# Performance work log

Measured on AMD Instinct MI355X. Metric: run time of the kernel, lower is better.

Reference implementation:

```python
import jax, jax.numpy as jnp
import numpy as np
import math

EMBED_DIM = 1024
NUM_HEADS = 16
HEAD_DIM = EMBED_DIM // NUM_HEADS
SCALE = 1.0 / math.sqrt(HEAD_DIM)


def setup_inputs() -> dict:
    key = jax.random.key(0)
    ks = jax.random.split(key, 11)
    B, S, E = 4, 2048, EMBED_DIM
    lim = 1.0 / math.sqrt(E)
    def lin(k):
        kw, kb = jax.random.split(k)
        W = jax.random.uniform(kw, (E, E), jnp.float32, -lim, lim)
        b = jax.random.uniform(kb, (E,), jnp.float32, -lim, lim)
        return W, b
    Wq, bq = lin(ks[0])
    Wk, bk = lin(ks[1])
    Wv, bv = lin(ks[2])
    Wo, bo = lin(ks[3])
    query = jax.random.normal(ks[4], (B, S, E), jnp.float32)
    key_t = jax.random.normal(ks[5], (B, S, E), jnp.float32)
    value = jax.random.normal(ks[6], (B, S, E), jnp.float32)
    return {"query": query, "key": key_t, "value": value,
            "Wq": Wq, "bq": bq, "Wk": Wk, "bk": bk,
            "Wv": Wv, "bv": bv, "Wo": Wo, "bo": bo}


def reference(query, key, value, Wq, bq, Wk, bk, Wv, bv, Wo, bo):
    B, S, E = query.shape
    H, D = NUM_HEADS, HEAD_DIM
    # nn.Linear: x @ W^T + b; reshape to (B, H, S, D)
    def proj(x, W, b):
        return (x @ W.T + b).reshape(B, S, H, D).transpose(0, 2, 1, 3)
    q = proj(query, Wq, bq)
    k = proj(key, Wk, bk)
    v = proj(value, Wv, bv)
    scores = jnp.einsum('bhsd,bhtd->bhst', q, k) * SCALE  # [B,H,S,S]
    attn = jax.nn.softmax(scores, axis=-1)
    # dropout is identity in eval/reference mode
    attended = jnp.einsum('bhst,bhtd->bhsd', attn, v)
    attended = attended.transpose(0, 2, 1, 3).reshape(B, S, E)
    out = attended @ Wo.T + bo
    return out, attn
```

## Files before the change

### kernel.cpp

```cpp
#include <hip/hip_runtime.h>
#include <hip/hip_bf16.h>

typedef __attribute__((ext_vector_type(8))) short short8;
typedef __attribute__((ext_vector_type(4))) float f32x4;
typedef unsigned short u16;
typedef unsigned int u32;

#define AS1 __attribute__((address_space(1)))
#define AS3 __attribute__((address_space(3)))

__device__ __forceinline__ void cp16(const void* g, void* l) {
  __builtin_amdgcn_global_load_lds((const AS1 u32*)g, (AS3 u32*)l, 16, 0, 0);
}

__device__ __forceinline__ u16 f2bf(float x) {
  union { float f; unsigned u; } c; c.f = x;
  unsigned u = c.u;
  unsigned r = (u + 0x7fffu + ((u >> 16) & 1u)) >> 16;
  return (u16)r;
}

__device__ __forceinline__ u32 pk2bf(float a, float b) {
  __hip_bfloat162 h = __float22bfloat162_rn(float2{a, b});
  union { __hip_bfloat162 h; u32 u; } c; c.h = h; return c.u;
}

__device__ __forceinline__ short8 cvt8(float4 x0, float4 x1) {
  short8 v;
  v[0]=(short)f2bf(x0.x); v[1]=(short)f2bf(x0.y); v[2]=(short)f2bf(x0.z); v[3]=(short)f2bf(x0.w);
  v[4]=(short)f2bf(x1.x); v[5]=(short)f2bf(x1.y); v[6]=(short)f2bf(x1.z); v[7]=(short)f2bf(x1.w);
  return v;
}

__global__ __launch_bounds__(256) void cvt_all(
    const float* __restrict__ q, const float* __restrict__ k, const float* __restrict__ v,
    const float* __restrict__ wq, const float* __restrict__ wk,
    const float* __restrict__ wv, const float* __restrict__ wo,
    u16* __restrict__ Xb, u16* __restrict__ Wb)
{
  const int TOT = 3670016;
  for (int c = blockIdx.x * 256 + threadIdx.x; c < TOT; c += gridDim.x * 256) {
    const float* s; u16* d;
    if (c < 3145728) {
      int z = c >> 20, off = c & 1048575;
      s = ((z == 0) ? q : (z == 1) ? k : v) + (size_t)off * 8;
      d = Xb + (size_t)c * 8;
    } else {
      int wc = c - 3145728;
      int z = wc >> 17, off = wc & 131071;
      s = ((z == 0) ? wq : (z == 1) ? wk : (z == 2) ? wv : wo) + (size_t)off * 8;
      d = Wb + (size_t)wc * 8;
    }
    float4 a = ((const float4*)s)[0], b = ((const float4*)s)[1];
    *(short8*)d = cvt8(a, b);
  }
}

template<int SWAP>
__device__ __forceinline__ void gemm_core_bf16(const u16* __restrict__ A,
                                               const u16* __restrict__ B,
                                               u16* As, u16* Bs,
                                               f32x4 acc[4][4])
{
  const int tid = threadIdx.x;
  const int lane = tid & 63, wid = tid >> 6;
  const int lo = lane & 15, hi = lane >> 4;
  const int wr0 = (wid >> 1) * 64, wc0 = (wid & 1) * 64;

  for (int k0 = 0; k0 < 1024; k0 += 64) {
    __syncthreads();
#pragma unroll
    for (int it = 0; it < 4; ++it) {
      int idx = it * 256 + tid;
      int row = idx >> 3, slot = idx & 7;
      cp16(A + (size_t)row * 1024 + k0 + slot * 8, As + (size_t)idx * 8);
      cp16(B + (size_t)row * 1024 + k0 + slot * 8, Bs + (size_t)idx * 8);
    }
    __syncthreads();
#pragma unroll
    for (int kk = 0; kk < 2; ++kk) {
      short8 af[4], bfr[4];
      int slot = kk * 4 + hi;
#pragma unroll
      for (int i = 0; i < 4; ++i)
        af[i] = *(const short8*)(&As[(wr0 + i * 16 + lo) * 64 + slot * 8]);
#pragma unroll
      for (int j = 0; j < 4; ++j)
        bfr[j] = *(const short8*)(&Bs[(wc0 + j * 16 + lo) * 64 + slot * 8]);
#pragma unroll
      for (int i = 0; i < 4; ++i)
#pragma unroll
        for (int j = 0; j < 4; ++j)
          acc[i][j] = SWAP
            ? __builtin_amdgcn_mfma_f32_16x16x32_bf16(bfr[j], af[i], acc[i][j], 0, 0, 0)
            : __builtin_amdgcn_mfma_f32_16x16x32_bf16(af[i], bfr[j], acc[i][j], 0, 0, 0);
    }
  }
}

__global__ __launch_bounds__(256) void gemm_qkv(
    const u16* __restrict__ Xb, const u16* __restrict__ Wb,
    const float* __restrict__ bq, const float* __restrict__ bk, const float* __restrict__ bv,
    u16* __restrict__ Qh, u16* __restrict__ Kh, u16* __restrict__ Vt)
{
  __shared__ __align__(16) u16 As[128 * 64];
  __shared__ __align__(16) u16 Bs[128 * 64];
  const int bid = blockIdx.x;
  const int w = (bid & 7) * 192 + (bid >> 3);
  const int z = w / 512, r = w % 512;
  const int bm0 = (r >> 3) * 128, bn0 = (r & 7) * 128;
  const u16* A = Xb + (size_t)z * 8388608 + (size_t)bm0 * 1024;
  const u16* W = Wb + (size_t)z * 1048576 + (size_t)bn0 * 1024;
  const float* bias = (z == 0) ? bq : (z == 1) ? bk : bv;

  f32x4 acc[4][4] = {};
  if (z < 2) gemm_core_bf16<0>(A, W, As, Bs, acc);
  else       gemm_core_bf16<1>(A, W, As, Bs, acc);

  const int lane = threadIdx.x & 63, wid = threadIdx.x >> 6;
  const int lo = lane & 15, hi = lane >> 4;
  const int wr0 = (wid >> 1) * 64, wc0 = (wid & 1) * 64;

  if (z < 2) {
    u16* out = (z == 0) ? Qh : Kh;
    const float sc = (z == 0) ? 0.125f * 1.44269504088896f : 1.0f;
#pragma unroll
    for (int j = 0; j < 4; ++j) {
      int n = bn0 + wc0 + j * 16 + lo;
      float bb = bias[n];
      int h = n >> 6, d = n & 63;
#pragma unroll
      for (int i = 0; i < 4; ++i)
#pragma unroll
        for (int r2 = 0; r2 < 4; ++r2) {
          int m = bm0 + wr0 + i * 16 + hi * 4 + r2;
          int b = m >> 11, s = m & 2047;
          float v = (acc[i][j][r2] + bb) * sc;
          out[(((size_t)(b * 16 + h)) * 2048 + s) * 64 + d] = f2bf(v);
        }
    }
  } else {
#pragma unroll
    for (int j = 0; j < 4; ++j) {
#pragma unroll
      for (int r2 = 0; r2 < 4; ++r2) {
        int n = bn0 + wc0 + j * 16 + hi * 4 + r2;
        float bb = bias[n];
        int h = n >> 6, d = n & 63;
#pragma unroll
        for (int i = 0; i < 4; ++i) {
          int m = bm0 + wr0 + i * 16 + lo;
          int b = m >> 11, s = m & 2047;
          Vt[(((size_t)(b * 16 + h)) * 64 + d) * 2048 + s] = f2bf(acc[i][j][r2] + bb);
        }
      }
    }
  }
}

__global__ __launch_bounds__(256) void gemm_out(
    const u16* __restrict__ ATT, const u16* __restrict__ Wo,
    const float* __restrict__ bo, float* __restrict__ out)
{
  __shared__ __align__(16) u16 As[128 * 64];
  __shared__ __align__(16) u16 Bs[128 * 64];
  const int bid = blockIdx.x;
  const int w = (bid & 7) * 64 + (bid >> 3);
  const int bm0 = (w >> 3) * 128, bn0 = (w & 7) * 128;
  f32x4 acc[4][4] = {};
  gemm_core_bf16<0>(ATT + (size_t)bm0 * 1024, Wo + (size_t)bn0 * 1024, As, Bs, acc);

  const int lane = threadIdx.x & 63, wid = threadIdx.x >> 6;
  const int lo = lane & 15, hi = lane >> 4;
  const int wr0 = (wid >> 1) * 64, wc0 = (wid & 1) * 64;
#pragma unroll
  for (int j = 0; j < 4; ++j) {
    int n = bn0 + wc0 + j * 16 + lo;
    float bb = bo[n];
#pragma unroll
    for (int i = 0; i < 4; ++i)
#pragma unroll
      for (int r = 0; r < 4; ++r) {
        int m = bm0 + wr0 + i * 16 + hi * 4 + r;
        out[(size_t)m * 1024 + n] = acc[i][j][r] + bb;
      }
  }
}

#define C2 11.5415603f
__global__ __launch_bounds__(256) void attn_fused(
    const u16* __restrict__ Qh, const u16* __restrict__ Kh,
    const u16* __restrict__ Vt, float* __restrict__ attnOut,
    u16* __restrict__ ATT)
{
  __shared__ __align__(16) u16 Ks[64 * 64];
  __shared__ __align__(16) u16 Vs[64 * 64];
  __shared__ __align__(16) u16 Ps[64 * 64];
  const int tid = threadIdx.x, lane = tid & 63, wid = tid >> 6;
  const int lo = lane & 15, hi = lane >> 4;
  const int bid = blockIdx.x;
  const int xcd = bid & 7, idx = bid >> 3;
  const int bh = xcd * 8 + (idx >> 5);
  const int q0 = (idx & 31) * 64;
  const int wq0 = wid * 16;
  const int qr = wq0 + lo;

  const u16* Qg  = Qh + ((size_t)bh * 2048 + q0) * 64;
  const u16* Kg0 = Kh + (size_t)bh * 2048 * 64;
  const u16* Vg0 = Vt + (size_t)bh * 64 * 2048;

  short8 qa[2];
#pragma unroll
  for (int kk = 0; kk < 2; ++kk)
    qa[kk] = *(const short8*)(Qg + qr * 64 + (kk * 4 + hi) * 8);

  float lsum = 0.f;
  for (int kt2 = 0; kt2 < 16; ++kt2) {
    int t0 = kt2 * 128;
    __syncthreads();
#pragma unroll
    for (int it = 0; it < 4; ++it) {
      int i2 = it * 256 + tid;
      int row = i2 >> 3, slot = i2 & 7;
      short8 v = *(const short8*)(Kg0 + (size_t)(t0 + row) * 64 + slot * 8);
      if (it < 2) *(short8*)(&Ks[row * 64 + ((slot ^ (row & 7)) << 3)]) = v;
      else        *(short8*)(&Vs[(row - 64) * 64 + ((slot ^ (row & 7)) << 3)]) = v;
    }
    __syncthreads();
#pragma unroll
    for (int half = 0; half < 2; ++half) {
      const u16* Kb = half ? Vs : Ks;
      f32x4 sc[4] = {};
#pragma unroll
      for (int kk = 0; kk < 2; ++kk) {
        int slot = kk * 4 + hi;
#pragma unroll
        for (int j = 0; j < 4; ++j) {
          int row = j * 16 + lo;
          short8 kb = *(const short8*)(&Kb[row * 64 + ((slot ^ (row & 7)) << 3)]);
          sc[j] = __builtin_amdgcn_mfma_f32_16x16x32_bf16(kb, qa[kk], sc[j], 0, 0, 0);
        }
      }
#pragma unroll
      for (int j = 0; j < 4; ++j)
#pragma unroll
        for (int r = 0; r < 4; ++r) lsum += __builtin_amdgcn_exp2f(sc[j][r] - C2);
    }
  }
  lsum += __shfl_xor(lsum, 16);
  lsum += __shfl_xor(lsum, 32);
  const float shift2 = C2 + __builtin_amdgcn_logf(lsum);

  f32x4 oacc[4] = {};
  for (int kt = 0; kt < 32; ++kt) {
    int t0 = kt * 64;
    __syncthreads();
#pragma unroll
    for (int it = 0; it < 2; ++it) {
      int i2 = it * 256 + tid;
      int row = i2 >> 3, slot = i2 & 7;
      short8 v = *(const short8*)(Kg0 + (size_t)(t0 + row) * 64 + slot * 8);
      *(short8*)(&Ks[row * 64 + ((slot ^ (row & 7)) << 3)]) = v;
      short8 w = *(const short8*)(Vg0 + (size_t)row * 2048 + t0 + slot * 8);
      *(short8*)(&Vs[row * 64 + ((slot ^ (row & 7)) << 3)]) = w;
    }
    __syncthreads();
    f32x4 sc[4] = {};
#pragma unroll
    for (int kk = 0; kk < 2; ++kk) {
      int slot = kk * 4 + hi;
#pragma unroll
      for (int j = 0; j < 4; ++j) {
        int row = j * 16 + lo;
        short8 kb = *(const short8*)(&Ks[row * 64 + ((slot ^ (row & 7)) << 3)]);
        sc[j] = __builtin_amdgcn_mfma_f32_16x16x32_bf16(kb, qa[kk], sc[j], 0, 0, 0);
      }
    }
    float p[4][4];
#pragma unroll
    for (int j = 0; j < 4; ++j)
#pragma unroll
      for (int r = 0; r < 4; ++r) p[j][r] = __builtin_amdgcn_exp2f(sc[j][r] - shift2);

    float* aOut = attnOut + ((size_t)bh * 2048 + q0 + qr) * 2048 + t0 + hi * 4;
#pragma unroll
    for (int j = 0; j < 4; ++j) {
      f32x4 f4;
      f4[0] = p[j][0]; f4[1] = p[j][1]; f4[2] = p[j][2]; f4[3] = p[j][3];
      __builtin_nontemporal_store(f4, (f32x4*)(aOut + j * 16));
    }
#pragma unroll
    for (int j = 0; j < 4; ++j) {
      int byte = (qr * 128 + j * 32 + hi * 8) ^ ((qr & 7) << 4);
      uint2 uu; uu.x = pk2bf(p[j][0], p[j][1]); uu.y = pk2bf(p[j][2], p[j][3]);
      *(uint2*)((char*)Ps + byte) = uu;
    }
#pragma unroll
    for (int c = 0; c < 2; ++c) {
      int byte = (qr * 128 + c * 64 + hi * 16) ^ ((qr & 7) << 4);
      short8 pa = *(const short8*)((char*)Ps + byte);
      int slot = c * 4 + hi;
#pragma unroll
      for (int j = 0; j < 4; ++j) {
        int vrow = j * 16 + lo;
        short8 vb = *(const short8*)(&Vs[vrow * 64 + ((slot ^ (vrow & 7)) << 3)]);
        oacc[j] = __builtin_amdgcn_mfma_f32_16x16x32_bf16(pa, vb, oacc[j], 0, 0, 0);
      }
    }
  }
  const int b = bh >> 4, h = bh & 15;
#pragma unroll
  for (int j = 0; j < 4; ++j)
#pragma unroll
    for (int r = 0; r < 4; ++r) {
      int ql = wq0 + hi * 4 + r;
      int d = j * 16 + lo;
      size_t row = (size_t)b * 2048 + q0 + ql;
      ATT[row * 1024 + h * 64 + d] = f2bf(oacc[j][r]);
    }
}

extern "C" void kernel_launch(void* const* d_in, const int* in_sizes, int n_in,
                              void* d_out, int out_size, void* d_ws, size_t ws_size,
                              hipStream_t stream) {
  const float* query = (const float*)d_in[0];
  const float* key   = (const float*)d_in[1];
  const float* value = (const float*)d_in[2];
  const float* Wq = (const float*)d_in[3];
  const float* bq = (const float*)d_in[4];
  const float* Wk = (const float*)d_in[5];
  const float* bk = (const float*)d_in[6];
  const float* Wv = (const float*)d_in[7];
  const float* bv = (const float*)d_in[8];
  const float* Wo = (const float*)d_in[9];
  const float* bo = (const float*)d_in[10];

  u16* Xb  = (u16*)d_ws;
  u16* Wb  = Xb + 25165824;
  u16* Qh  = Wb + 4194304;
  u16* Kh  = Qh + 8388608;
  u16* Vt  = Kh + 8388608;
  u16* ATT = Xb;

  float* outO  = (float*)d_out;
  float* attnO = outO + (size_t)8388608;

  cvt_all<<<2048, 256, 0, stream>>>(query, key, value, Wq, Wk, Wv, Wo, Xb, Wb);
  gemm_qkv<<<1536, 256, 0, stream>>>(Xb, Wb, bq, bk, bv, Qh, Kh, Vt);
  attn_fused<<<2048, 256, 0, stream>>>(Qh, Kh, Vt, attnO, ATT);
  gemm_out<<<512, 256, 0, stream>>>(ATT, Wb + 3145728, bo, outO);
}
```

Measured before the change: 460.7 us.

## Double-buffer K/V tiles in LDS with register prefetch in attention kernel

Both attention passes now keep two LDS buffers for the K and V tiles. The next tile is loaded from global memory into registers before the current tile's MFMA work and written to the other buffer afterward, so each iteration needs one barrier instead of two. This overlaps global load latency with compute. In exchange it doubles LDS for K/V and raises register pressure, which may lower occupancy; the first pass also moves from 128-key steps to 64-key steps.

```diff
diff --git a/kernel.cpp b/kernel.cpp
--- a/kernel.cpp
+++ b/kernel.cpp
@@ -193,8 +193,8 @@
     const u16* __restrict__ Vt, float* __restrict__ attnOut,
     u16* __restrict__ ATT)
 {
-  __shared__ __align__(16) u16 Ks[64 * 64];
-  __shared__ __align__(16) u16 Vs[64 * 64];
+  __shared__ __align__(16) u16 Ks[2][64 * 64];
+  __shared__ __align__(16) u16 Vs[2][64 * 64];
   __shared__ __align__(16) u16 Ps[64 * 64];
   const int tid = threadIdx.x, lane = tid & 63, wid = tid >> 6;
   const int lo = lane & 15, hi = lane >> 4;
@@ -209,62 +209,78 @@
   const u16* Kg0 = Kh + (size_t)bh * 2048 * 64;
   const u16* Vg0 = Vt + (size_t)bh * 64 * 2048;
 
+  const int srow0 = tid >> 3,         sslot0 = tid & 7;
+  const int srow1 = (256 + tid) >> 3, sslot1 = tid & 7;
+  const int dst0 = srow0 * 64 + ((sslot0 ^ (srow0 & 7)) << 3);
+  const int dst1 = srow1 * 64 + ((sslot1 ^ (srow1 & 7)) << 3);
+
   short8 qa[2];
 #pragma unroll
   for (int kk = 0; kk < 2; ++kk)
     qa[kk] = *(const short8*)(Qg + qr * 64 + (kk * 4 + hi) * 8);
 
+  {
+    short8 k0 = *(const short8*)(Kg0 + (size_t)srow0 * 64 + sslot0 * 8);
+    short8 k1 = *(const short8*)(Kg0 + (size_t)srow1 * 64 + sslot1 * 8);
+    *(short8*)(&Ks[0][dst0]) = k0;
+    *(short8*)(&Ks[0][dst1]) = k1;
+  }
+  __syncthreads();
   float lsum = 0.f;
-  for (int kt2 = 0; kt2 < 16; ++kt2) {
-    int t0 = kt2 * 128;
+  for (int kt = 0; kt < 32; ++kt) {
+    const int cur = kt & 1;
+    short8 kn0, kn1;
+    if (kt < 31) {
+      const u16* Kn = Kg0 + (size_t)(kt + 1) * 4096;
+      kn0 = *(const short8*)(Kn + (size_t)srow0 * 64 + sslot0 * 8);
+      kn1 = *(const short8*)(Kn + (size_t)srow1 * 64 + sslot1 * 8);
+    }
+    f32x4 sc[4] = {};
+#pragma unroll
+    for (int kk = 0; kk < 2; ++kk) {
+      int slot = kk * 4 + hi;
+#pragma unroll
+      for (int j = 0; j < 4; ++j) {
+        int row = j * 16 + lo;
+        short8 kb = *(const short8*)(&Ks[cur][row * 64 + ((slot ^ (row & 7)) << 3)]);
+        sc[j] = __builtin_amdgcn_mfma_f32_16x16x32_bf16(kb, qa[kk], sc[j], 0, 0, 0);
+      }
+    }
+#pragma unroll
+    for (int j = 0; j < 4; ++j)
+#pragma unroll
+      for (int r = 0; r < 4; ++r) lsum += __builtin_amdgcn_exp2f(sc[j][r] - C2);
+    if (kt < 31) {
+      *(short8*)(&Ks[cur ^ 1][dst0]) = kn0;
+      *(short8*)(&Ks[cur ^ 1][dst1]) = kn1;
+    }
     __syncthreads();
-#pragma unroll
-    for (int it = 0; it < 4; ++it) {
-      int i2 = it * 256 + tid;
-      int row = i2 >> 3, slot = i2 & 7;
-      short8 v = *(const short8*)(Kg0 + (size_t)(t0 + row) * 64 + slot * 8);
-      if (it < 2) *(short8*)(&Ks[row * 64 + ((slot ^ (row & 7)) << 3)]) = v;
-      else        *(short8*)(&Vs[(row - 64) * 64 + ((slot ^ (row & 7)) << 3)]) = v;
-    }
-    __syncthreads();
-#pragma unroll
-    for (int half = 0; half < 2; ++half) {
-      const u16* Kb = half ? Vs : Ks;
-      f32x4 sc[4] = {};
-#pragma unroll
-      for (int kk = 0; kk < 2; ++kk) {
-        int slot = kk * 4 + hi;
-#pragma unroll
-        for (int j = 0; j < 4; ++j) {
-          int row = j * 16 + lo;
-          short8 kb = *(const short8*)(&Kb[row * 64 + ((slot ^ (row & 7)) << 3)]);
-          sc[j] = __builtin_amdgcn_mfma_f32_16x16x32_bf16(kb, qa[kk], sc[j], 0, 0, 0);
-        }
-      }
-#pragma unroll
-      for (int j = 0; j < 4; ++j)
-#pragma unroll
-        for (int r = 0; r < 4; ++r) lsum += __builtin_amdgcn_exp2f(sc[j][r] - C2);
-    }
   }
   lsum += __shfl_xor(lsum, 16);
   lsum += __shfl_xor(lsum, 32);
   const float shift2 = C2 + __builtin_amdgcn_logf(lsum);
 
+  {
+    short8 k0 = *(const short8*)(Kg0 + (size_t)srow0 * 64 + sslot0 * 8);
+    short8 k1 = *(const short8*)(Kg0 + (size_t)srow1 * 64 + sslot1 * 8);
+    short8 v0 = *(const short8*)(Vg0 + (size_t)srow0 * 2048 + sslot0 * 8);
+    short8 v1 = *(const short8*)(Vg0 + (size_t)srow1 * 2048 + sslot1 * 8);
+    *(short8*)(&Ks[0][dst0]) = k0;  *(short8*)(&Ks[0][dst1]) = k1;
+    *(short8*)(&Vs[0][dst0]) = v0;  *(short8*)(&Vs[0][dst1]) = v1;
+  }
+  __syncthreads();
   f32x4 oacc[4] = {};
   for (int kt = 0; kt < 32; ++kt) {
-    int t0 = kt * 64;
-    __syncthreads();
-#pragma unroll
-    for (int it = 0; it < 2; ++it) {
-      int i2 = it * 256 + tid;
-      int row = i2 >> 3, slot = i2 & 7;
-      short8 v = *(const short8*)(Kg0 + (size_t)(t0 + row) * 64 + slot * 8);
-      *(short8*)(&Ks[row * 64 + ((slot ^ (row & 7)) << 3)]) = v;
-      short8 w = *(const short8*)(Vg0 + (size_t)row * 2048 + t0 + slot * 8);
-      *(short8*)(&Vs[row * 64 + ((slot ^ (row & 7)) << 3)]) = w;
-    }
-    __syncthreads();
+    const int cur = kt & 1;
+    const int t0 = kt * 64;
+    short8 kn0, kn1, vn0, vn1;
+    if (kt < 31) {
+      const u16* Kn = Kg0 + (size_t)(kt + 1) * 4096;
+      kn0 = *(const short8*)(Kn + (size_t)srow0 * 64 + sslot0 * 8);
+      kn1 = *(const short8*)(Kn + (size_t)srow1 * 64 + sslot1 * 8);
+      vn0 = *(const short8*)(Vg0 + (size_t)srow0 * 2048 + (t0 + 64) + sslot0 * 8);
+      vn1 = *(const short8*)(Vg0 + (size_t)srow1 * 2048 + (t0 + 64) + sslot1 * 8);
+    }
     f32x4 sc[4] = {};
 #pragma unroll
     for (int kk = 0; kk < 2; ++kk) {
@@ -272,7 +288,7 @@
 #pragma unroll
       for (int j = 0; j < 4; ++j) {
         int row = j * 16 + lo;
-        short8 kb = *(const short8*)(&Ks[row * 64 + ((slot ^ (row & 7)) << 3)]);
+        short8 kb = *(const short8*)(&Ks[cur][row * 64 + ((slot ^ (row & 7)) << 3)]);
         sc[j] = __builtin_amdgcn_mfma_f32_16x16x32_bf16(kb, qa[kk], sc[j], 0, 0, 0);
       }
     }
@@ -303,10 +319,17 @@
 #pragma unroll
       for (int j = 0; j < 4; ++j) {
         int vrow = j * 16 + lo;
-        short8 vb = *(const short8*)(&Vs[vrow * 64 + ((slot ^ (vrow & 7)) << 3)]);
+        short8 vb = *(const short8*)(&Vs[cur][vrow * 64 + ((slot ^ (vrow & 7)) << 3)]);
         oacc[j] = __builtin_amdgcn_mfma_f32_16x16x32_bf16(pa, vb, oacc[j], 0, 0, 0);
       }
     }
+    if (kt < 31) {
+      *(short8*)(&Ks[cur ^ 1][dst0]) = kn0;
+      *(short8*)(&Ks[cur ^ 1][dst1]) = kn1;
+      *(short8*)(&Vs[cur ^ 1][dst0]) = vn0;
+      *(short8*)(&Vs[cur ^ 1][dst1]) = vn1;
+    }
+    __syncthreads();
   }
   const int b = bh >> 4, h = bh & 15;
 #pragma unroll
```

After: 439.5 us. 4.6% less time.
